# Kernel tuning notes

Measured on AMD Instinct MI355X. Metric: run time of the kernel, lower is better.

Reference implementation:

```python
import jax, jax.numpy as jnp
import numpy as np

EMBED = 1024

def setup_inputs() -> dict:
    key = jax.random.key(0)
    ks = jax.random.split(key, 10)
    B, S, E = 4, 2048, EMBED
    inv = 1.0 / np.sqrt(E)
    return {
        "query": jax.random.normal(ks[0], (B, S, E), jnp.float32),
        "key": jax.random.normal(ks[1], (B, S, E), jnp.float32),
        "value": jax.random.normal(ks[2], (B, S, E), jnp.float32),
        "attn_mask": jnp.zeros((B, S, S), jnp.float32),
        "Wq": jax.random.normal(ks[3], (E, E), jnp.float32) * inv,
        "bq": jnp.zeros((E,), jnp.float32),
        "Wk": jax.random.normal(ks[4], (E, E), jnp.float32) * inv,
        "bk": jnp.zeros((E,), jnp.float32),
        "Wv": jax.random.normal(ks[5], (E, E), jnp.float32) * inv,
        "bv": jnp.zeros((E,), jnp.float32),
    }

def reference(query, key, value, attn_mask, Wq, bq, Wk, bk, Wv, bv):
    E = query.shape[-1]
    q = query @ Wq.T + bq            # [B,S,E]
    k = key @ Wk.T + bk              # [B,S,E]
    v = value @ Wv.T + bv            # [B,S,E]
    scores = jnp.einsum('bse,bte->bst', q, k) / jnp.sqrt(jnp.float32(E))
    scores = scores + attn_mask      # [B,S,S]
    attn = jax.nn.softmax(scores, axis=-1)
    return jnp.einsum('bst,bte->bse', attn, v)
```

## Files before the change

### kernel.cpp

```cpp
#include <hip/hip_runtime.h>
#include <cstdint>
#include <cstddef>

typedef __bf16 bf16;
typedef __bf16 bf16x8 __attribute__((ext_vector_type(8)));
typedef float  f32x4  __attribute__((ext_vector_type(4)));

#define NB 4
#define SS 2048
#define EE 1024

#define BUFB  24576
#define LDS3  (3 * BUFB)

static __device__ __forceinline__ void glds16(const bf16* g, void* l)
{
    __builtin_amdgcn_global_load_lds(
        (const __attribute__((address_space(1))) unsigned int*)g,
        (__attribute__((address_space(3))) unsigned int*)l,
        16, 0, 0);
}

static __device__ __forceinline__ void swz_block(int& bx, int& by, int& bz)
{
    const int nx = gridDim.x, ny = gridDim.y;
    const int nwg = nx * ny * gridDim.z;
    int lin = blockIdx.x + nx * (blockIdx.y + ny * blockIdx.z);
    const int per = nwg >> 3;
    lin = (lin & 7) * per + (lin >> 3);
    bz = lin / (nx * ny);
    const int r = lin - bz * nx * ny;
    by = r / nx;
    bx = r - by * nx;
}

static __device__ __forceinline__ void kloop32(
    const bf16* __restrict__ A, const bf16* __restrict__ Bm,
    int lda, int ldb, int nt, char* lds, int m0, int n0, int tid,
    f32x4 acc[4][4])
{
    constexpr int NBUF = 3;
    const int lane = tid & 63, w = tid >> 6;
    const int wm = w >> 2, wn = w & 3;
    const int lr = lane & 15, kq = lane >> 4;
    const int cb = ((kq ^ ((lr >> 1) & 3)) << 4);

    const int srow   = tid >> 2;
    const int chunkL = (tid & 3) ^ ((srow >> 1) & 3);
    const bf16* Asrc = A  + (size_t)(m0 + srow) * lda + chunkL * 8;
    const bf16* Bsrc = Bm + (size_t)(n0 + srow) * ldb + chunkL * 8;
    const int wofs = w << 10;

#pragma unroll
    for (int p = 0; p < NBUF - 1; ++p) {
        char* d = lds + p * BUFB + wofs;
        const int kt = p * 32;
        glds16(Asrc + kt,                     d);
        glds16(Bsrc + kt,                     d + 8192);
        glds16(Bsrc + (size_t)128 * ldb + kt, d + 16384);
    }
    asm volatile("s_waitcnt vmcnt(3)" ::: "memory");
    __builtin_amdgcn_sched_barrier(0);
    __builtin_amdgcn_s_barrier();
    __builtin_amdgcn_sched_barrier(0);

    int rb = 0, sb = NBUF - 1;
    for (int t = 0; t < nt; ++t) {
        char* la = lds + rb * BUFB;
        char* lb = la + 8192;
        const int ts = (t + NBUF - 1 < nt) ? t + NBUF - 1 : nt - 1;
        const int kt = ts * 32;
        char* d = lds + sb * BUFB + wofs;

        bf16x8 af[4], bg[4];
#pragma unroll
        for (int m = 0; m < 4; ++m)
            af[m] = *(const bf16x8*)(la + (wm * 64 + m * 16 + lr) * 64 + cb);
#pragma unroll
        for (int n = 0; n < 4; ++n)
            bg[n] = *(const bf16x8*)(lb + (wn * 64 + n * 16 + lr) * 64 + cb);

        glds16(Asrc + kt,                     d);
        glds16(Bsrc + kt,                     d + 8192);
        glds16(Bsrc + (size_t)128 * ldb + kt, d + 16384);

        __builtin_amdgcn_s_setprio(1);
#pragma unroll
        for (int m = 0; m < 4; ++m)
#pragma unroll
            for (int n = 0; n < 4; ++n)
                acc[m][n] = __builtin_amdgcn_mfma_f32_16x16x32_bf16(af[m], bg[n], acc[m][n], 0, 0, 0);
        __builtin_amdgcn_s_setprio(0);

        if (t < nt - 1) {
            asm volatile("s_waitcnt vmcnt(3)" ::: "memory");
            __builtin_amdgcn_sched_barrier(0);
            __builtin_amdgcn_s_barrier();
            __builtin_amdgcn_sched_barrier(0);
        }
        rb = (rb + 1 == NBUF) ? 0 : rb + 1;
        sb = (sb + 1 == NBUF) ? 0 : sb + 1;
    }
    asm volatile("s_waitcnt vmcnt(0)" ::: "memory");
}

__global__ __launch_bounds__(256) void cvt_all(
    const float* __restrict__ q, const float* __restrict__ k, const float* __restrict__ v,
    const float* __restrict__ Wq, const float* __restrict__ Wk, const float* __restrict__ Wv,
    bf16* __restrict__ qc, bf16* __restrict__ kc, bf16* __restrict__ vc,
    bf16* __restrict__ Wc)
{
    const int y = blockIdx.y;
    const float* s; bf16* d; size_t i;
    if (blockIdx.x < 4096) {
        s = (y == 0) ? q : (y == 1) ? k : v;
        d = (y == 0) ? qc : (y == 1) ? kc : vc;
        i = ((size_t)blockIdx.x * 256 + threadIdx.x) * 8;
    } else {
        s = (y == 0) ? Wq : (y == 1) ? Wk : Wv;
        d = Wc + (size_t)y * EE * EE;
        i = ((size_t)(blockIdx.x - 4096) * 256 + threadIdx.x) * 8;
    }
    const float4 f0 = *(const float4*)(s + i);
    const float4 f1 = *(const float4*)(s + i + 4);
    bf16x8 h;
    h[0] = (bf16)f0.x; h[1] = (bf16)f0.y; h[2] = (bf16)f0.z; h[3] = (bf16)f0.w;
    h[4] = (bf16)f1.x; h[5] = (bf16)f1.y; h[6] = (bf16)f1.z; h[7] = (bf16)f1.w;
    *(bf16x8*)(d + i) = h;
}

__global__ __launch_bounds__(512, 4) void proj8(
    const bf16* __restrict__ qc, const bf16* __restrict__ kc, const bf16* __restrict__ vc,
    const bf16* __restrict__ Wc,
    const float* __restrict__ bq, const float* __restrict__ bk, const float* __restrict__ bv,
    bf16* __restrict__ qb, bf16* __restrict__ kb, bf16* __restrict__ vb)
{
    extern __shared__ char lds[];
    int bx, by, bz; swz_block(bx, by, bz);
    const bf16* A; const float* bias; bf16* out;
    if (bz == 0)      { A = qc; bias = bq; out = qb; }
    else if (bz == 1) { A = kc; bias = bk; out = kb; }
    else              { A = vc; bias = bv; out = vb; }
    const bf16* Bm = Wc + (size_t)bz * EE * EE;

    const int m0 = by * 128, n0 = bx * 256;
    const int tid = threadIdx.x;

    f32x4 acc[4][4];
#pragma unroll
    for (int m = 0; m < 4; ++m)
#pragma unroll
        for (int n = 0; n < 4; ++n) { acc[m][n][0] = 0.f; acc[m][n][1] = 0.f; acc[m][n][2] = 0.f; acc[m][n][3] = 0.f; }

    kloop32(A, Bm, EE, EE, EE / 32, lds, m0, n0, tid, acc);

    const int lane = tid & 63, w = tid >> 6, wm = w >> 2, wn = w & 3;
    const int lr = lane & 15, kq = lane >> 4;
#pragma unroll
    for (int n = 0; n < 4; ++n) {
        const int gcol = n0 + wn * 64 + n * 16 + lr;
        const float bb = bias[gcol];
#pragma unroll
        for (int m = 0; m < 4; ++m)
#pragma unroll
            for (int j = 0; j < 4; ++j) {
                const int grow = m0 + wm * 64 + m * 16 + kq * 4 + j;
                out[(size_t)grow * EE + gcol] = (bf16)(acc[m][n][j] + bb);
            }
    }
}

__global__ __launch_bounds__(256) void transpose_kernel(const bf16* __restrict__ vb,
                                                        bf16* __restrict__ vt)
{
    __shared__ bf16 t[64][72];
    const int b  = blockIdx.z;
    const int s0 = blockIdx.x * 64, e0 = blockIdx.y * 64;
    const int tid = threadIdx.x;

    const bf16* src = vb + ((size_t)b * SS + s0) * EE + e0;
#pragma unroll
    for (int i = 0; i < 2; ++i) {
        const int c  = tid * 2 + i;
        const int r  = c >> 3;
        const int cc = (c & 7) * 8;
        *(uint4*)&t[r][cc] = *(const uint4*)&src[(size_t)r * EE + cc];
    }
    __syncthreads();

    bf16* dst = vt + ((size_t)b * EE + e0) * SS + s0;
    const int er  = tid >> 2;
    const int sc0 = (tid & 3) * 16;
    bf16 tmp[16];
#pragma unroll
    for (int k2 = 0; k2 < 16; ++k2) tmp[k2] = t[sc0 + k2][er];
    *(uint4*)&dst[(size_t)er * SS + sc0]     = *(uint4*)&tmp[0];
    *(uint4*)&dst[(size_t)er * SS + sc0 + 8] = *(uint4*)&tmp[8];
}

__global__ __launch_bounds__(512, 4) void scores8(const bf16* __restrict__ qb,
                                                  const bf16* __restrict__ kb,
                                                  const float* __restrict__ mask,
                                                  bf16* __restrict__ sc)
{
    extern __shared__ char lds[];
    int bx, by, bz; swz_block(bx, by, bz);
    const bf16* A  = qb + (size_t)bz * SS * EE;
    const bf16* Bm = kb + (size_t)bz * SS * EE;

    const int m0 = by * 128, n0 = bx * 256;
    const int tid = threadIdx.x;

    f32x4 acc[4][4];
#pragma unroll
    for (int m = 0; m < 4; ++m)
#pragma unroll
        for (int n = 0; n < 4; ++n) { acc[m][n][0] = 0.f; acc[m][n][1] = 0.f; acc[m][n][2] = 0.f; acc[m][n][3] = 0.f; }

    kloop32(A, Bm, EE, EE, EE / 32, lds, m0, n0, tid, acc);

    const int lane = tid & 63, w = tid >> 6, wm = w >> 2, wn = w & 3;
    const int lr = lane & 15, kq = lane >> 4;
    const float* mrow = mask + (size_t)bz * SS * SS;
    bf16* out = sc + (size_t)bz * SS * SS;
    const float scale = 0.03125f;
#pragma unroll
    for (int m = 0; m < 4; ++m)
#pragma unroll
        for (int n = 0; n < 4; ++n)
#pragma unroll
            for (int j = 0; j < 4; ++j) {
                const int grow = m0 + wm * 64 + m * 16 + kq * 4 + j;
                const int gcol = n0 + wn * 64 + n * 16 + lr;
                const float v = acc[m][n][j] * scale + mrow[(size_t)grow * SS + gcol];
                out[(size_t)grow * SS + gcol] = (bf16)v;
            }
}

__global__ __launch_bounds__(256) void softmax_kernel(bf16* __restrict__ sc)
{
    __shared__ float red[4];
    const size_t row = blockIdx.x;
    uint4* rp = (uint4*)(sc + row * (size_t)SS);
    const int tid = threadIdx.x, lane = tid & 63, wid = tid >> 6;

    const uint4 d = rp[tid];
    const unsigned int u[4] = { d.x, d.y, d.z, d.w };
    float f[8];
#pragma unroll
    for (int i = 0; i < 4; ++i) {
        union { unsigned int i_; float f_; } lo, hi;
        lo.i_ = u[i] << 16;
        hi.i_ = u[i] & 0xffff0000u;
        f[2 * i]     = lo.f_;
        f[2 * i + 1] = hi.f_;
    }

    float m = f[0];
#pragma unroll
    for (int i = 1; i < 8; ++i) m = fmaxf(m, f[i]);
#pragma unroll
    for (int o = 32; o > 0; o >>= 1) m = fmaxf(m, __shfl_xor(m, o));
    if (lane == 0) red[wid] = m;
    __syncthreads();
    m = fmaxf(fmaxf(red[0], red[1]), fmaxf(red[2], red[3]));
    __syncthreads();

    float e[8], s = 0.f;
#pragma unroll
    for (int i = 0; i < 8; ++i) { e[i] = __expf(f[i] - m); s += e[i]; }
#pragma unroll
    for (int o = 32; o > 0; o >>= 1) s += __shfl_xor(s, o);
    if (lane == 0) red[wid] = s;
    __syncthreads();
    s = red[0] + red[1] + red[2] + red[3];
    const float inv = 1.0f / s;

    unsigned int ou[4];
#pragma unroll
    for (int i = 0; i < 4; ++i) {
        union { bf16 h; unsigned short b; } a0, a1;
        a0.h = (bf16)(e[2 * i] * inv);
        a1.h = (bf16)(e[2 * i + 1] * inv);
        ou[i] = ((unsigned int)a1.b << 16) | (unsigned int)a0.b;
    }
    rp[tid] = make_uint4(ou[0], ou[1], ou[2], ou[3]);
}

__global__ __launch_bounds__(512, 4) void pv8(const bf16* __restrict__ sc,
                                              const bf16* __restrict__ vt,
                                              float* __restrict__ outp)
{
    extern __shared__ char lds[];
    int bx, by, bz; swz_block(bx, by, bz);
    const bf16* A  = sc + (size_t)bz * SS * SS;
    const bf16* Bm = vt + (size_t)bz * EE * SS;

    const int m0 = by * 128, n0 = bx * 256;
    const int tid = threadIdx.x;

    f32x4 acc[4][4];
#pragma unroll
    for (int m = 0; m < 4; ++m)
#pragma unroll
        for (int n = 0; n < 4; ++n) { acc[m][n][0] = 0.f; acc[m][n][1] = 0.f; acc[m][n][2] = 0.f; acc[m][n][3] = 0.f; }

    kloop32(A, Bm, SS, SS, SS / 32, lds, m0, n0, tid, acc);

    const int lane = tid & 63, w = tid >> 6, wm = w >> 2, wn = w & 3;
    const int lr = lane & 15, kq = lane >> 4;
#pragma unroll
    for (int m = 0; m < 4; ++m)
#pragma unroll
        for (int n = 0; n < 4; ++n)
#pragma unroll
            for (int j = 0; j < 4; ++j) {
                const int grow = m0 + wm * 64 + m * 16 + kq * 4 + j;
                const int gcol = n0 + wn * 64 + n * 16 + lr;
                outp[((size_t)bz * SS + grow) * EE + gcol] = acc[m][n][j];
            }
}

extern "C" void kernel_launch(void* const* d_in, const int* in_sizes, int n_in,
                              void* d_out, int out_size, void* d_ws, size_t ws_size,
                              hipStream_t stream)
{
    const float* query = (const float*)d_in[0];
    const float* key_  = (const float*)d_in[1];
    const float* value = (const float*)d_in[2];
    const float* mask  = (const float*)d_in[3];
    const float* Wq = (const float*)d_in[4];
    const float* bq = (const float*)d_in[5];
    const float* Wk = (const float*)d_in[6];
    const float* bk = (const float*)d_in[7];
    const float* Wv = (const float*)d_in[8];
    const float* bv = (const float*)d_in[9];
    float* outp = (float*)d_out;

    char* ws = (char*)d_ws;
    const size_t QKV = (size_t)NB * SS * EE * 2;
    const size_t SCB = (size_t)NB * SS * SS * 2;
    const size_t WCB = (size_t)3 * EE * EE * 2;
    if (ws_size < 4 * QKV + SCB + WCB) return;

    bf16* qb = (bf16*)(ws);
    bf16* kb = (bf16*)(ws + QKV);
    bf16* vb = (bf16*)(ws + 2 * QKV);
    bf16* vt = (bf16*)(ws + 3 * QKV);
    bf16* sc = (bf16*)(ws + 4 * QKV);
    bf16* Wc = (bf16*)(ws + 4 * QKV + SCB);
    bf16* qc = vt;
    bf16* kc = sc;
    bf16* vc = (bf16*)(ws + 5 * QKV);

    (void)hipFuncSetAttribute((const void*)proj8,   hipFuncAttributeMaxDynamicSharedMemorySize, LDS3);
    (void)hipFuncSetAttribute((const void*)scores8, hipFuncAttributeMaxDynamicSharedMemorySize, LDS3);
    (void)hipFuncSetAttribute((const void*)pv8,     hipFuncAttributeMaxDynamicSharedMemorySize, LDS3);

    dim3 blk(256), blk5(512);
    cvt_all<<<dim3(4096 + 512, 3), blk, 0, stream>>>(
        query, key_, value, Wq, Wk, Wv, qc, kc, vc, Wc);

    proj8<<<dim3(EE / 256, (NB * SS) / 128, 3), blk5, LDS3, stream>>>(
        qc, kc, vc, Wc, bq, bk, bv, qb, kb, vb);
    transpose_kernel<<<dim3(SS / 64, EE / 64, NB), blk, 0, stream>>>(vb, vt);
    scores8<<<dim3(SS / 256, SS / 128, NB), blk5, LDS3, stream>>>(qb, kb, mask, sc);
    softmax_kernel<<<dim3(NB * SS), blk, 0, stream>>>(sc);
    pv8<<<dim3(EE / 256, SS / 128, NB), blk5, LDS3, stream>>>(sc, vt, outp);
}
```

Baseline: 203.7 us.

## Fuse V transpose into projection epilogue and use 64-wide K tiles in PV GEMM

The V projection epilogue now stages its output tile through LDS and writes it already transposed into vt, so the separate transpose kernel and the vb intermediate are dropped. This removes one launch and a full read and write of V. Separately, the PV GEMM switches to a new k-loop with 64-wide K tiles and triple-buffered LDS (144 KB). That halves the barrier count per tile but drops the occupancy hint and allows fewer resident workgroups per CU.

```diff
diff --git a/kernel.cpp b/kernel.cpp
--- a/kernel.cpp
+++ b/kernel.cpp
@@ -10,8 +10,10 @@
 #define SS 2048
 #define EE 1024
 
-#define BUFB  24576
-#define LDS3  (3 * BUFB)
+#define BUFB   24576
+#define LDS3   (3 * BUFB)
+#define BUFB64 49152
+#define LDS64  (3 * BUFB64)
 
 static __device__ __forceinline__ void glds16(const bf16* g, void* l)
 {
@@ -102,6 +104,98 @@
         sb = (sb + 1 == NBUF) ? 0 : sb + 1;
     }
     asm volatile("s_waitcnt vmcnt(0)" ::: "memory");
+}
+
+static __device__ __forceinline__ void kloop64(
+    const bf16* __restrict__ A, const bf16* __restrict__ Bm,
+    int lda, int ldb, int nt, char* lds, int m0, int n0, int tid,
+    f32x4 acc[4][4])
+{
+    const int lane = tid & 63, w = tid >> 6;
+    const int wm = w >> 2, wn = w & 3;
+    const int lr = lane & 15, kq = lane >> 4;
+    const int axor = (lr & 7) << 4;
+
+    const int srow   = tid >> 3;
+    const int chunkL = (tid & 7) ^ (srow & 7);
+    const bf16* Asrc = A  + (size_t)(m0 + srow) * lda + chunkL * 8;
+    const bf16* Bsrc = Bm + (size_t)(n0 + srow) * ldb + chunkL * 8;
+    const int wofs = w << 10;
+
+#pragma unroll
+    for (int p = 0; p < 2; ++p) {
+        char* d = lds + p * BUFB64 + wofs;
+        const int kt = p * 64;
+        glds16(Asrc + kt,                        d);
+        glds16(Asrc + (size_t)64 * lda + kt,     d + 8192);
+        glds16(Bsrc + kt,                        d + 16384);
+        glds16(Bsrc + (size_t)64 * ldb + kt,     d + 16384 + 8192);
+        glds16(Bsrc + (size_t)128 * ldb + kt,    d + 16384 + 16384);
+        glds16(Bsrc + (size_t)192 * ldb + kt,    d + 16384 + 24576);
+    }
+    asm volatile("s_waitcnt vmcnt(6)" ::: "memory");
+    __builtin_amdgcn_sched_barrier(0);
+    __builtin_amdgcn_s_barrier();
+    __builtin_amdgcn_sched_barrier(0);
+
+    for (int t = 0; t < nt; ++t) {
+        char* la = lds + (t % 3) * BUFB64;
+        char* lb = la + 16384;
+        char* sa = lds + ((t + 2) % 3) * BUFB64;
+        const bool st = (t + 2) < nt;
+        const int kt = (t + 2) * 64;
+
+        bf16x8 af[4], bg[4];
+        {
+            const int cbk = (kq * 16) ^ axor;
+#pragma unroll
+            for (int m = 0; m < 4; ++m)
+                af[m] = *(const bf16x8*)(la + (wm * 64 + m * 16 + lr) * 128 + cbk);
+#pragma unroll
+            for (int n = 0; n < 4; ++n)
+                bg[n] = *(const bf16x8*)(lb + (wn * 64 + n * 16 + lr) * 128 + cbk);
+            if (st) {
+                glds16(Asrc + kt,                    sa + wofs);
+                glds16(Asrc + (size_t)64 * lda + kt, sa + 8192 + wofs);
+                glds16(Bsrc + kt,                    sa + 16384 + wofs);
+            }
+            __builtin_amdgcn_s_setprio(1);
+#pragma unroll
+            for (int m = 0; m < 4; ++m)
+#pragma unroll
+                for (int n = 0; n < 4; ++n)
+                    acc[m][n] = __builtin_amdgcn_mfma_f32_16x16x32_bf16(af[m], bg[n], acc[m][n], 0, 0, 0);
+            __builtin_amdgcn_s_setprio(0);
+        }
+        {
+            const int cbk = (64 + kq * 16) ^ axor;
+#pragma unroll
+            for (int m = 0; m < 4; ++m)
+                af[m] = *(const bf16x8*)(la + (wm * 64 + m * 16 + lr) * 128 + cbk);
+#pragma unroll
+            for (int n = 0; n < 4; ++n)
+                bg[n] = *(const bf16x8*)(lb + (wn * 64 + n * 16 + lr) * 128 + cbk);
+            if (st) {
+                glds16(Bsrc + (size_t)64 * ldb + kt,  sa + 16384 + 8192 + wofs);
+                glds16(Bsrc + (size_t)128 * ldb + kt, sa + 16384 + 16384 + wofs);
+                glds16(Bsrc + (size_t)192 * ldb + kt, sa + 16384 + 24576 + wofs);
+            }
+            __builtin_amdgcn_s_setprio(1);
+#pragma unroll
+            for (int m = 0; m < 4; ++m)
+#pragma unroll
+                for (int n = 0; n < 4; ++n)
+                    acc[m][n] = __builtin_amdgcn_mfma_f32_16x16x32_bf16(af[m], bg[n], acc[m][n], 0, 0, 0);
+            __builtin_amdgcn_s_setprio(0);
+        }
+        if (t < nt - 1) {
+            if (st) { asm volatile("s_waitcnt vmcnt(6)" ::: "memory"); }
+            else    { asm volatile("s_waitcnt vmcnt(0)" ::: "memory"); }
+            __builtin_amdgcn_sched_barrier(0);
+            __builtin_amdgcn_s_barrier();
+            __builtin_amdgcn_sched_barrier(0);
+        }
+    }
 }
 
 __global__ __launch_bounds__(256) void cvt_all(
@@ -133,14 +227,14 @@
     const bf16* __restrict__ qc, const bf16* __restrict__ kc, const bf16* __restrict__ vc,
     const bf16* __restrict__ Wc,
     const float* __restrict__ bq, const float* __restrict__ bk, const float* __restrict__ bv,
-    bf16* __restrict__ qb, bf16* __restrict__ kb, bf16* __restrict__ vb)
+    bf16* __restrict__ qb, bf16* __restrict__ kb, bf16* __restrict__ vt)
 {
     extern __shared__ char lds[];
     int bx, by, bz; swz_block(bx, by, bz);
-    const bf16* A; const float* bias; bf16* out;
-    if (bz == 0)      { A = qc; bias = bq; out = qb; }
-    else if (bz == 1) { A = kc; bias = bk; out = kb; }
-    else              { A = vc; bias = bv; out = vb; }
+    const bf16* A; const float* bias;
+    if (bz == 0)      { A = qc; bias = bq; }
+    else if (bz == 1) { A = kc; bias = bk; }
+    else              { A = vc; bias = bv; }
     const bf16* Bm = Wc + (size_t)bz * EE * EE;
 
     const int m0 = by * 128, n0 = bx * 256;
@@ -156,46 +250,53 @@
 
     const int lane = tid & 63, w = tid >> 6, wm = w >> 2, wn = w & 3;
     const int lr = lane & 15, kq = lane >> 4;
-#pragma unroll
-    for (int n = 0; n < 4; ++n) {
-        const int gcol = n0 + wn * 64 + n * 16 + lr;
-        const float bb = bias[gcol];
-#pragma unroll
-        for (int m = 0; m < 4; ++m)
-#pragma unroll
-            for (int j = 0; j < 4; ++j) {
-                const int grow = m0 + wm * 64 + m * 16 + kq * 4 + j;
-                out[(size_t)grow * EE + gcol] = (bf16)(acc[m][n][j] + bb);
+
+    if (bz < 2) {
+        bf16* out = (bz == 0) ? qb : kb;
+#pragma unroll
+        for (int n = 0; n < 4; ++n) {
+            const int gcol = n0 + wn * 64 + n * 16 + lr;
+            const float bb = bias[gcol];
+#pragma unroll
+            for (int m = 0; m < 4; ++m)
+#pragma unroll
+                for (int j = 0; j < 4; ++j) {
+                    const int grow = m0 + wm * 64 + m * 16 + kq * 4 + j;
+                    out[(size_t)grow * EE + gcol] = (bf16)(acc[m][n][j] + bb);
+                }
+        }
+    } else {
+        __syncthreads();
+#pragma unroll
+        for (int n = 0; n < 4; ++n) {
+            const int gc = wn * 64 + n * 16 + lr;
+            const float bb = bias[n0 + gc];
+#pragma unroll
+            for (int m = 0; m < 4; ++m) {
+                const int gr = wm * 64 + m * 16 + kq * 4;
+                union { unsigned short u[4]; uint2 v; } h;
+#pragma unroll
+                for (int j = 0; j < 4; ++j) {
+                    union { bf16 b; unsigned short u; } cv;
+                    cv.b = (bf16)(acc[m][n][j] + bb);
+                    h.u[j] = cv.u;
+                }
+                char* p = lds + gc * 256 + (((gr >> 3) ^ (gc & 7)) << 4) + (gr & 7) * 2;
+                *(uint2*)p = h.v;
             }
-    }
-}
-
-__global__ __launch_bounds__(256) void transpose_kernel(const bf16* __restrict__ vb,
-                                                        bf16* __restrict__ vt)
-{
-    __shared__ bf16 t[64][72];
-    const int b  = blockIdx.z;
-    const int s0 = blockIdx.x * 64, e0 = blockIdx.y * 64;
-    const int tid = threadIdx.x;
-
-    const bf16* src = vb + ((size_t)b * SS + s0) * EE + e0;
-#pragma unroll
-    for (int i = 0; i < 2; ++i) {
-        const int c  = tid * 2 + i;
-        const int r  = c >> 3;
-        const int cc = (c & 7) * 8;
-        *(uint4*)&t[r][cc] = *(const uint4*)&src[(size_t)r * EE + cc];
-    }
-    __syncthreads();
-
-    bf16* dst = vt + ((size_t)b * EE + e0) * SS + s0;
-    const int er  = tid >> 2;
-    const int sc0 = (tid & 3) * 16;
-    bf16 tmp[16];
-#pragma unroll
-    for (int k2 = 0; k2 < 16; ++k2) tmp[k2] = t[sc0 + k2][er];
-    *(uint4*)&dst[(size_t)er * SS + sc0]     = *(uint4*)&tmp[0];
-    *(uint4*)&dst[(size_t)er * SS + sc0 + 8] = *(uint4*)&tmp[8];
+        }
+        __syncthreads();
+        const int r = tid >> 1, par = tid & 1;
+        const int bb_ = m0 >> 11;
+        const int s0 = m0 & (SS - 1);
+        bf16* dst = vt + ((size_t)bb_ * EE + n0 + r) * SS + s0 + par * 64;
+#pragma unroll
+        for (int i = 0; i < 8; ++i) {
+            const int c = par * 8 + i;
+            const char* p = lds + r * 256 + ((c ^ (r & 7)) << 4);
+            *(uint4*)&dst[i * 8] = *(const uint4*)p;
+        }
+    }
 }
 
 __global__ __launch_bounds__(512, 4) void scores8(const bf16* __restrict__ qb,
@@ -287,9 +388,9 @@
     rp[tid] = make_uint4(ou[0], ou[1], ou[2], ou[3]);
 }
 
-__global__ __launch_bounds__(512, 4) void pv8(const bf16* __restrict__ sc,
-                                              const bf16* __restrict__ vt,
-                                              float* __restrict__ outp)
+__global__ __launch_bounds__(512) void pv8(const bf16* __restrict__ sc,
+                                           const bf16* __restrict__ vt,
+                                           float* __restrict__ outp)
 {
     extern __shared__ char lds[];
     int bx, by, bz; swz_block(bx, by, bz);
@@ -305,7 +406,7 @@
 #pragma unroll
         for (int n = 0; n < 4; ++n) { acc[m][n][0] = 0.f; acc[m][n][1] = 0.f; acc[m][n][2] = 0.f; acc[m][n][3] = 0.f; }
 
-    kloop32(A, Bm, SS, SS, SS / 32, lds, m0, n0, tid, acc);
+    kloop64(A, Bm, SS, SS, SS / 64, lds, m0, n0, tid, acc);
 
     const int lane = tid & 63, w = tid >> 6, wm = w >> 2, wn = w & 3;
     const int lr = lane & 15, kq = lane >> 4;
@@ -345,26 +446,24 @@
 
     bf16* qb = (bf16*)(ws);
     bf16* kb = (bf16*)(ws + QKV);
-    bf16* vb = (bf16*)(ws + 2 * QKV);
     bf16* vt = (bf16*)(ws + 3 * QKV);
     bf16* sc = (bf16*)(ws + 4 * QKV);
     bf16* Wc = (bf16*)(ws + 4 * QKV + SCB);
-    bf16* qc = vt;
+    bf16* qc = (bf16*)(ws + 2 * QKV);
     bf16* kc = sc;
     bf16* vc = (bf16*)(ws + 5 * QKV);
 
     (void)hipFuncSetAttribute((const void*)proj8,   hipFuncAttributeMaxDynamicSharedMemorySize, LDS3);
     (void)hipFuncSetAttribute((const void*)scores8, hipFuncAttributeMaxDynamicSharedMemorySize, LDS3);
-    (void)hipFuncSetAttribute((const void*)pv8,     hipFuncAttributeMaxDynamicSharedMemorySize, LDS3);
+    (void)hipFuncSetAttribute((const void*)pv8,     hipFuncAttributeMaxDynamicSharedMemorySize, LDS64);
 
     dim3 blk(256), blk5(512);
     cvt_all<<<dim3(4096 + 512, 3), blk, 0, stream>>>(
         query, key_, value, Wq, Wk, Wv, qc, kc, vc, Wc);
 
     proj8<<<dim3(EE / 256, (NB * SS) / 128, 3), blk5, LDS3, stream>>>(
-        qc, kc, vc, Wc, bq, bk, bv, qb, kb, vb);
-    transpose_kernel<<<dim3(SS / 64, EE / 64, NB), blk, 0, stream>>>(vb, vt);
+        qc, kc, vc, Wc, bq, bk, bv, qb, kb, vt);
     scores8<<<dim3(SS / 256, SS / 128, NB), blk5, LDS3, stream>>>(qb, kb, mask, sc);
     softmax_kernel<<<dim3(NB * SS), blk, 0, stream>>>(sc);
-    pv8<<<dim3(EE / 256, SS / 128, NB), blk5, LDS3, stream>>>(sc, vt, outp);
-}
+    pv8<<<dim3(EE / 256, SS / 128, NB), blk5, LDS64, stream>>>(sc, vt, outp);
+}
```

After: 194.2 us, median of 2. 1.05x faster.
